# Kernel tuning notes

Measured on AMD Instinct MI355X. Metric: run time of the kernel, lower is better.

The kernel has to match this reference:

```python
import jax, jax.numpy as jnp
import numpy as np

WS = 14  # window size
NH = 12  # num heads
EPS = 1e-5  # torch LayerNorm eps


def _rel_idx(ws: int) -> np.ndarray:
    coords = np.stack(np.meshgrid(np.arange(ws), np.arange(ws), indexing='ij'))
    cf = coords.reshape(2, -1)                      # (2, N)
    rel = cf[:, :, None] - cf[:, None, :]           # (2, N, N)
    rel = rel.transpose(1, 2, 0).copy()
    rel[:, :, 0] += ws - 1
    rel[:, :, 1] += ws - 1
    rel[:, :, 0] *= 2 * ws - 1
    return rel.sum(-1)                              # (N, N) int


def _layernorm(x, w, b):
    mu = jnp.mean(x, axis=-1, keepdims=True)
    var = jnp.var(x, axis=-1, keepdims=True)
    return (x - mu) * jax.lax.rsqrt(var + EPS) * w + b


def setup_inputs() -> dict:
    key = jax.random.key(0)
    ks = jax.random.split(key, 8)
    d, dff = 768, 3072
    s = lambda k, shape, sc: jax.random.normal(k, shape, jnp.float32) * sc
    return {
        'x': jax.random.normal(ks[0], (8, d, 56, 56), jnp.float32),
        'norm1_w': jnp.ones((d,), jnp.float32),
        'norm1_b': jnp.zeros((d,), jnp.float32),
        'qkv_w': s(ks[1], (d, 3 * d), 0.02),
        'qkv_b': jnp.zeros((3 * d,), jnp.float32),
        'rel_bias_table': s(ks[2], ((2 * WS - 1) ** 2, NH), 0.02),
        'proj_w': s(ks[3], (d, d), 0.02),
        'proj_b': jnp.zeros((d,), jnp.float32),
        'norm2_w': jnp.ones((d,), jnp.float32),
        'norm2_b': jnp.zeros((d,), jnp.float32),
        'fc1_w': s(ks[4], (d, dff), 0.02),
        'fc1_b': jnp.zeros((dff,), jnp.float32),
        'fc2_w': s(ks[5], (dff, d), 0.02),
        'fc2_b': jnp.zeros((d,), jnp.float32),
        'gamma1': jnp.full((d,), 1e-5, jnp.float32),
        'gamma2': jnp.full((d,), 1e-5, jnp.float32),
    }


def reference(x, norm1_w, norm1_b, qkv_w, qkv_b, rel_bias_table, proj_w, proj_b,
              norm2_w, norm2_b, fc1_w, fc1_b, fc2_w, fc2_b, gamma1, gamma2):
    B, C, H, W = x.shape
    nh, hd = NH, C // NH
    N = WS * WS
    xs = jnp.transpose(x, (0, 2, 3, 1))             # B,H,W,C
    shortcut = xs
    h = _layernorm(xs, norm1_w, norm1_b)

    # window partition (H, W divisible by WS)
    hw = h.reshape(B, H // WS, WS, W // WS, WS, C)
    hw = jnp.transpose(hw, (0, 1, 3, 2, 4, 5)).reshape(-1, N, C)  # (Bw, N, C)

    qkv = hw @ qkv_w + qkv_b                        # (Bw, N, 3C)
    qkv = qkv.reshape(-1, N, 3, nh, hd)
    q, k, v = [jnp.transpose(qkv[:, :, i], (0, 2, 1, 3)) for i in range(3)]  # (Bw,nh,N,hd)

    attn = jnp.einsum('bhnd,bhmd->bhnm', q, k) * (hd ** -0.5)
    rel_idx = jnp.asarray(_rel_idx(WS))             # static (N,N)
    bias = rel_bias_table[rel_idx]                  # (N,N,nh)
    attn = attn + jnp.transpose(bias, (2, 0, 1))[None]
    attn = jax.nn.softmax(attn, axis=-1)

    out = jnp.einsum('bhnm,bhmd->bnhd', attn, v).reshape(-1, N, C)
    out = out @ proj_w + proj_b                     # (Bw, N, C)

    # window reverse
    out = out.reshape(B, H // WS, W // WS, WS, WS, C)
    out = jnp.transpose(out, (0, 1, 3, 2, 4, 5)).reshape(B, H, W, C)

    xs = shortcut + gamma1 * out
    h2 = _layernorm(xs, norm2_w, norm2_b)
    mlp = jax.nn.gelu(h2 @ fc1_w + fc1_b, approximate=False) @ fc2_w + fc2_b
    xs = xs + gamma2 * mlp
    return jnp.transpose(xs, (0, 3, 1, 2))          # B,C,H,W
```

## Files before the change

kernel.cpp:

```cpp
#include <hip/hip_runtime.h>
#include <cstdint>
#include <cstddef>


typedef unsigned short u16;
typedef short short8 __attribute__((ext_vector_type(8)));
typedef float floatx4 __attribute__((ext_vector_type(4)));

static __device__ __forceinline__ float bf2f(u16 u) {
  return __uint_as_float(((unsigned)u) << 16);
}
static __device__ __forceinline__ u16 f2bf(float f) {
  unsigned u = __float_as_uint(f);
  return (u16)((u + 0x7FFFu + ((u >> 16) & 1u)) >> 16);
}
static __device__ __forceinline__ float ldin(const void* p, size_t i, int isf) {
  return isf ? ((const float*)p)[i] : bf2f(((const u16*)p)[i]);
}
static __device__ __forceinline__ void gload_lds16(const void* g, void* l) {
  __builtin_amdgcn_global_load_lds(
      (const __attribute__((address_space(1))) void*)g,
      (__attribute__((address_space(3))) void*)l, 16, 0, 0);
}
static __device__ __forceinline__ float fast_gelu(float v) {
  float u2 = v * (1.5957691216f + 0.0713548163f * v * v);
  return v * (1.0f / (1.0f + __expf(-u2)));
}

__global__ __launch_bounds__(256) void detect_kernel(const u16* __restrict__ x,
                                                     int* __restrict__ flag) {
  __shared__ int tot;
  if (threadIdx.x == 0) tot = 0;
  __syncthreads();
  int cnt = 0;
  for (int i = threadIdx.x; i < 4096; i += 256) {
    int e = (x[i] >> 7) & 0xFF;
    if (e >= 0xC1) cnt++;
  }
  atomicAdd(&tot, cnt);
  __syncthreads();
  if (threadIdx.x == 0) flag[0] = (tot > 16) ? 1 : 0;
}

__global__ __launch_bounds__(256) void cvt_params_kernel(
    const void* n1w, const void* n1b, const void* qkvb, const void* projb,
    const void* n2w, const void* n2b, const void* fc1b, const void* fc2b,
    const void* g1, const void* g2, const void* bt, u16* __restrict__ P,
    const int* __restrict__ flag) {
  int isf = *flag;
  int i = blockIdx.x * 256 + threadIdx.x;
  const void* src; int off;
  if      (i < 768)   { src = n1w;   off = i; }
  else if (i < 1536)  { src = n1b;   off = i - 768; }
  else if (i < 3840)  { src = qkvb;  off = i - 1536; }
  else if (i < 4608)  { src = projb; off = i - 3840; }
  else if (i < 5376)  { src = n2w;   off = i - 4608; }
  else if (i < 6144)  { src = n2b;   off = i - 5376; }
  else if (i < 9216)  { src = fc1b;  off = i - 6144; }
  else if (i < 9984)  { src = fc2b;  off = i - 9216; }
  else if (i < 10752) { src = g1;    off = i - 9984; }
  else if (i < 11520) { src = g2;    off = i - 10752; }
  else if (i < 20268) { src = bt;    off = i - 11520; }
  else return;
  P[i] = f2bf(ldin(src, off, isf));
}

__global__ __launch_bounds__(256) void wtr_kernel(const void* __restrict__ W,
                                                  u16* __restrict__ WT,
                                                  int K, int N,
                                                  const int* __restrict__ flag) {
  int isf = *flag;
  __shared__ u16 tl[32][33];
  int tx = threadIdx.x, ty = threadIdx.y;
  int n0 = blockIdx.x * 32, k0 = blockIdx.y * 32;
#pragma unroll
  for (int j = 0; j < 32; j += 8)
    tl[ty + j][tx] = f2bf(ldin(W, (size_t)(k0 + ty + j) * N + n0 + tx, isf));
  __syncthreads();
#pragma unroll
  for (int j = 0; j < 32; j += 8)
    WT[(size_t)(n0 + ty + j) * K + k0 + tx] = tl[tx][ty + j];
}

__global__ __launch_bounds__(256) void tin_kernel(const void* __restrict__ x,
                                                  u16* __restrict__ sc,
                                                  const int* __restrict__ flag) {
  int isf = *flag;
  int cc = blockIdx.x, h = blockIdx.y, b = blockIdx.z;
  __shared__ u16 tile[64 * 57];
  int tid = threadIdx.x;
  for (int i = tid; i < 64 * 56; i += 256) {
    int ci = i / 56, w = i - ci * 56;
    tile[ci * 57 + w] =
        f2bf(ldin(x, (((size_t)b * 768 + cc * 64 + ci) * 56 + h) * 56 + w, isf));
  }
  __syncthreads();
  int hb = h / 14, hi = h - hb * 14;
  for (int i = tid; i < 56 * 64; i += 256) {
    int w = i >> 6, ci = i & 63;
    int wb = w / 14, wj = w - wb * 14;
    int r = (b * 16 + hb * 4 + wb) * 196 + hi * 14 + wj;
    sc[(size_t)r * 768 + cc * 64 + ci] = tile[ci * 57 + w];
  }
}

__global__ __launch_bounds__(256) void tout_kernel(const u16* __restrict__ src,
                                                   void* __restrict__ out,
                                                   const int* __restrict__ flag) {
  int isf = *flag;
  int cc = blockIdx.x, h = blockIdx.y, b = blockIdx.z;
  __shared__ u16 tile[64 * 57];
  int tid = threadIdx.x;
  int hb = h / 14, hi = h - hb * 14;
  for (int i = tid; i < 56 * 64; i += 256) {
    int w = i >> 6, ci = i & 63;
    int wb = w / 14, wj = w - wb * 14;
    int r = (b * 16 + hb * 4 + wb) * 196 + hi * 14 + wj;
    tile[ci * 57 + w] = src[(size_t)r * 768 + cc * 64 + ci];
  }
  __syncthreads();
  for (int i = tid; i < 64 * 56; i += 256) {
    int ci = i / 56, w = i - ci * 56;
    size_t o = (((size_t)b * 768 + cc * 64 + ci) * 56 + h) * 56 + w;
    if (isf) ((float*)out)[o] = bf2f(tile[ci * 57 + w]);
    else     ((u16*)out)[o]   = tile[ci * 57 + w];
  }
}

__global__ __launch_bounds__(256) void ln_kernel(const u16* __restrict__ xin,
                                                 const u16* __restrict__ wt,
                                                 const u16* __restrict__ bs,
                                                 u16* __restrict__ out) {
  int row = blockIdx.x, t = threadIdx.x;
  const u16* xr = xin + (size_t)row * 768;
  float v0 = bf2f(xr[t]), v1 = bf2f(xr[t + 256]), v2 = bf2f(xr[t + 512]);
  float s1 = v0 + v1 + v2;
  float s2 = v0 * v0 + v1 * v1 + v2 * v2;
#pragma unroll
  for (int off = 32; off > 0; off >>= 1) {
    s1 += __shfl_xor(s1, off);
    s2 += __shfl_xor(s2, off);
  }
  __shared__ float p1[4], p2[4];
  if ((t & 63) == 0) { p1[t >> 6] = s1; p2[t >> 6] = s2; }
  __syncthreads();
  float S1 = p1[0] + p1[1] + p1[2] + p1[3];
  float S2 = p2[0] + p2[1] + p2[2] + p2[3];
  float mu = S1 * (1.f / 768.f);
  float var = S2 * (1.f / 768.f) - mu * mu;
  float rs = rsqrtf(var + 1e-5f);
  u16* orow = out + (size_t)row * 768;
  orow[t]       = f2bf((v0 - mu) * rs * bf2f(wt[t])       + bf2f(bs[t]));
  orow[t + 256] = f2bf((v1 - mu) * rs * bf2f(wt[t + 256]) + bf2f(bs[t + 256]));
  orow[t + 512] = f2bf((v2 - mu) * rs * bf2f(wt[t + 512]) + bf2f(bs[t + 512]));
}

template <int EPI, int NPH>
__global__ __launch_bounds__(512, 2) void gemm256_kernel(
    const u16* __restrict__ A, const u16* __restrict__ BT,
    const u16* __restrict__ bias, const u16* __restrict__ gamma,
    u16* __restrict__ out, int M, int N, int K, int NX, int NYT) {
  constexpr int BN   = 64 * NPH;
  constexpr int WM   = 8 / NPH;
  constexpr int MF   = 2 * NPH;
  constexpr int ABUF = 8192;
  constexpr int BBUF = 2048 * NPH;
  constexpr int BUFSZ = ABUF + BBUF;
  __shared__ __align__(16) u16 LDS[4 * BUFSZ];

  int bid = blockIdx.x;
  int r8 = bid & 7, q = bid >> 3;
  int xb = q % NX, yb = (q / NX) * 8 + r8;
  if (yb >= NYT) return;
  int m0 = yb * 256, n0 = xb * BN;

  int tid = threadIdx.x;
  int w = tid >> 6, l = tid & 63;
  int l15 = l & 15, quad = l >> 4;
  int wm = w & (WM - 1), wn = w / WM;

  int lrow16 = l >> 2;
  int lk = ((l & 3) ^ ((l >> 3) & 3)) * 8;
  int ra0 = m0 + w * 32 + lrow16;       if (ra0 > M - 1) ra0 = M - 1;
  int ra1 = m0 + w * 32 + 16 + lrow16;  if (ra1 > M - 1) ra1 = M - 1;
  const u16* a0 = A + (size_t)ra0 * K + lk;
  const u16* a1 = A + (size_t)ra1 * K + lk;
  const u16* b0;
  const u16* b1;
  int dB0, dB1;
  if constexpr (NPH == 4) {
    b0 = BT + (size_t)(n0 + w * 32 + lrow16) * K + lk;
    b1 = BT + (size_t)(n0 + w * 32 + 16 + lrow16) * K + lk;
    dB0 = (w * 2) * 512; dB1 = (w * 2 + 1) * 512;
  } else {
    b0 = BT + (size_t)(n0 + w * 16 + lrow16) * K + lk;
    b1 = b0; dB0 = w * 512; dB1 = 0;
  }
  int dA0 = (w * 2) * 512, dA1 = (w * 2 + 1) * 512;

  int kqs = (quad ^ ((l15 >> 1) & 3)) * 8;

  floatx4 acc[MF][4];
#pragma unroll
  for (int i = 0; i < MF; ++i)
#pragma unroll
    for (int jn = 0; jn < 4; ++jn)
#pragma unroll
      for (int e = 0; e < 4; ++e) acc[i][jn][e] = 0.f;

  int nt = K >> 5;

  auto STAGE = [&](int s) {
    u16* bb = LDS + (size_t)(s & 3) * BUFSZ;
    int ko = s << 5;
    gload_lds16(a0 + ko, bb + dA0);
    gload_lds16(a1 + ko, bb + dA1);
    gload_lds16(b0 + ko, bb + ABUF + dB0);
    if constexpr (NPH == 4) gload_lds16(b1 + ko, bb + ABUF + dB1);
  };

#pragma unroll
  for (int pt = 0; pt < 3; ++pt)
    if (pt < nt) STAGE(pt);

  for (int t = 0; t < nt; ++t) {
    int rem = nt - 1 - t;
    if constexpr (NPH == 4) {
      if (rem >= 2)      asm volatile("s_waitcnt vmcnt(8)" ::: "memory");
      else if (rem == 1) asm volatile("s_waitcnt vmcnt(4)" ::: "memory");
      else               asm volatile("s_waitcnt vmcnt(0)" ::: "memory");
    } else {
      if (rem >= 2)      asm volatile("s_waitcnt vmcnt(6)" ::: "memory");
      else if (rem == 1) asm volatile("s_waitcnt vmcnt(3)" ::: "memory");
      else               asm volatile("s_waitcnt vmcnt(0)" ::: "memory");
    }
    __builtin_amdgcn_s_barrier();
    if (t + 3 < nt) STAGE(t + 3);

    const u16* Ac = LDS + (size_t)(t & 3) * BUFSZ;
    const u16* Bc = Ac + ABUF;
    __builtin_amdgcn_s_setprio(1);
    short8 bfr[4];
#pragma unroll
    for (int ni = 0; ni < 4; ++ni)
      bfr[ni] = *(const short8*)&Bc[(wn * 64 + ni * 16 + l15) * 32 + kqs];
#pragma unroll
    for (int mi = 0; mi < MF; ++mi) {
      short8 afr =
          *(const short8*)&Ac[(wm * (32 * NPH) + mi * 16 + l15) * 32 + kqs];
#pragma unroll
      for (int ni = 0; ni < 4; ++ni)
        acc[mi][ni] = __builtin_amdgcn_mfma_f32_16x16x32_bf16(
            afr, bfr[ni], acc[mi][ni], 0, 0, 0);
    }
    __builtin_amdgcn_s_setprio(0);
  }

  constexpr int CSTR = BN + 8;
  u16* Cs = LDS;
  float bv[4];
#pragma unroll
  for (int ni = 0; ni < 4; ++ni)
    bv[ni] = bf2f(bias[n0 + wn * 64 + ni * 16 + l15]);
  for (int cch = 0; cch < 2; ++cch) {
    __syncthreads();
    if (((wm * NPH) >> 2) == cch) {
      int rbase = wm * (32 * NPH) - cch * 128 + quad * 4;
#pragma unroll
      for (int mi = 0; mi < MF; ++mi)
#pragma unroll
        for (int ni = 0; ni < 4; ++ni) {
          int cl = wn * 64 + ni * 16 + l15;
#pragma unroll
          for (int reg = 0; reg < 4; ++reg) {
            float v = acc[mi][ni][reg] + bv[ni];
            if constexpr (EPI == 2) v = fast_gelu(v);
            Cs[(rbase + mi * 16 + reg) * CSTR + cl] = f2bf(v);
          }
        }
    }
    __syncthreads();
#pragma unroll
    for (int it = 0; it < BN / 32; ++it) {
      int idx = it * 512 + tid;
      int row = idx / (BN / 8);
      int c8 = (idx - row * (BN / 8)) * 8;
      int grow = m0 + cch * 128 + row;
      if (grow < M) {
        short8 val = *(const short8*)&Cs[row * CSTR + c8];
        u16* po = out + (size_t)grow * N + n0 + c8;
        if constexpr (EPI == 1) {
          short8 rv = *(const short8*)po;
          short8 gv = *(const short8*)(gamma + n0 + c8);
          short8 res;
#pragma unroll
          for (int e = 0; e < 8; ++e)
            res[e] = (short)f2bf(bf2f((u16)rv[e]) +
                                 bf2f((u16)gv[e]) * bf2f((u16)val[e]));
          *(short8*)po = res;
        } else {
          *(short8*)po = val;
        }
      }
    }
  }
}

__global__ __launch_bounds__(256) void attn_kernel(const u16* __restrict__ qkv,
                                                   const u16* __restrict__ btab,
                                                   u16* __restrict__ out) {
  __shared__ __align__(16) u16 VT[64 * 232];
  __shared__ __align__(16) u16 Pa[4 * 2 * 512];
  __shared__ float bS[729];
  int bid = blockIdx.x;
  int win = bid / 12, h = bid - win * 12;
  int tid = threadIdx.x, w = tid >> 6, l = tid & 63;
  int lane15 = l & 15, quad = l >> 4;
  const u16* qbase = qkv + (size_t)win * 196 * 2304;

  for (int i = tid; i < 64 * 28; i += 256) {
    int d = i / 28, m = i - d * 28;
    VT[d * 232 + 196 + m] = 0;
  }
  for (int i = tid; i < 196 * 64; i += 256) {
    int m = i >> 6, d = i & 63;
    VT[d * 232 + m] = qbase[(size_t)m * 2304 + 1536 + h * 64 + d];
  }
  for (int i = tid; i < 729; i += 256) bS[i] = bf2f(btab[i * 12 + h]);
  __syncthreads();

  u16* Pw = Pa + w * 1024;
  for (int rt = w; rt < 13; rt += 4) {
    floatx4 acc[13];
#pragma unroll
    for (int nt = 0; nt < 13; ++nt)
#pragma unroll
      for (int e = 0; e < 4; ++e) acc[nt][e] = 0.f;

    int rq = rt * 16 + lane15;
    bool qok = rq < 196;
#pragma unroll
    for (int kk = 0; kk < 2; ++kk) {
      short8 qf;
      if (qok)
        qf = *(const short8*)&qbase[(size_t)rq * 2304 + h * 64 + kk * 32 + quad * 8];
      else
#pragma unroll
        for (int e = 0; e < 8; ++e) qf[e] = 0;
#pragma unroll
      for (int nt = 0; nt < 13; ++nt) {
        int n = nt * 16 + lane15;
        short8 kf = *(const short8*)&qbase[(size_t)n * 2304 + 768 + h * 64 + kk * 32 + quad * 8];
        acc[nt] = __builtin_amdgcn_mfma_f32_16x16x32_bf16(qf, kf, acc[nt], 0, 0, 0);
      }
    }

    int i1[4], j1[4]; bool rv[4]; float mx[4], sm[4];
#pragma unroll
    for (int reg = 0; reg < 4; ++reg) {
      int r = rt * 16 + quad * 4 + reg;
      i1[reg] = r / 14; j1[reg] = r - i1[reg] * 14;
      rv[reg] = r < 196; mx[reg] = -1e30f; sm[reg] = 0.f;
    }
#pragma unroll
    for (int nt = 0; nt < 13; ++nt) {
      int cc = nt * 16 + lane15;
      bool cv = cc < 196;
      int i2 = cc / 14, j2 = cc - i2 * 14;
#pragma unroll
      for (int reg = 0; reg < 4; ++reg) {
        float v;
        if (cv) {
          v = acc[nt][reg] * 0.125f;
          if (rv[reg]) v += bS[(i1[reg] - i2 + 13) * 27 + (j1[reg] - j2 + 13)];
        } else v = -1e30f;
        acc[nt][reg] = v;
        mx[reg] = fmaxf(mx[reg], v);
      }
    }
#pragma unroll
    for (int reg = 0; reg < 4; ++reg)
#pragma unroll
      for (int off = 1; off < 16; off <<= 1)
        mx[reg] = fmaxf(mx[reg], __shfl_xor(mx[reg], off));
#pragma unroll
    for (int nt = 0; nt < 13; ++nt)
#pragma unroll
      for (int reg = 0; reg < 4; ++reg) {
        float p = __expf(acc[nt][reg] - mx[reg]);
        acc[nt][reg] = p; sm[reg] += p;
      }
#pragma unroll
    for (int reg = 0; reg < 4; ++reg) {
#pragma unroll
      for (int off = 1; off < 16; off <<= 1) sm[reg] += __shfl_xor(sm[reg], off);
      sm[reg] = 1.f / sm[reg];
    }

    floatx4 oa[4];
#pragma unroll
    for (int dt = 0; dt < 4; ++dt)
#pragma unroll
      for (int e = 0; e < 4; ++e) oa[dt][e] = 0.f;
#pragma unroll
    for (int kk = 0; kk < 7; ++kk) {
      u16* Pb = Pw + (kk & 1) * 512;
#pragma unroll
      for (int p = 0; p < 2; ++p) {
        int nt = kk * 2 + p;
#pragma unroll
        for (int reg = 0; reg < 4; ++reg) {
          float v = (nt < 13) ? acc[nt][reg] * sm[reg] : 0.f;
          Pb[(quad * 4 + reg) * 32 + p * 16 + lane15] = f2bf(v);
        }
      }
      asm volatile("s_waitcnt lgkmcnt(0)" ::: "memory");
      short8 pf = *(const short8*)&Pb[lane15 * 32 + quad * 8];
#pragma unroll
      for (int dt = 0; dt < 4; ++dt) {
        short8 vf = *(const short8*)&VT[(dt * 16 + lane15) * 232 + kk * 32 + quad * 8];
        oa[dt] = __builtin_amdgcn_mfma_f32_16x16x32_bf16(pf, vf, oa[dt], 0, 0, 0);
      }
    }
#pragma unroll
    for (int dt = 0; dt < 4; ++dt)
#pragma unroll
      for (int reg = 0; reg < 4; ++reg) {
        int r = rt * 16 + quad * 4 + reg;
        if (r < 196)
          out[((size_t)win * 196 + r) * 768 + h * 64 + dt * 16 + lane15] =
              f2bf(oa[dt][reg]);
      }
  }
}

static inline int gemm_grid(int NX, int NYT) { return NX * ((NYT + 7) / 8) * 8; }

extern "C" void kernel_launch(void* const* d_in, const int* in_sizes, int n_in,
                              void* d_out, int out_size, void* d_ws, size_t ws_size,
                              hipStream_t stream) {
  const void* x      = d_in[0];
  const void* n1w    = d_in[1];
  const void* n1b    = d_in[2];
  const void* qkv_w  = d_in[3];
  const void* qkv_b  = d_in[4];
  const void* btab   = d_in[5];
  const void* proj_w = d_in[6];
  const void* proj_b = d_in[7];
  const void* n2w    = d_in[8];
  const void* n2b    = d_in[9];
  const void* fc1_w  = d_in[10];
  const void* fc1_b  = d_in[11];
  const void* fc2_w  = d_in[12];
  const void* fc2_b  = d_in[13];
  const void* gamma1 = d_in[14];
  const void* gamma2 = d_in[15];
  (void)in_sizes; (void)n_in; (void)out_size;

  int c;
  if      (ws_size >= 245432576ull) c = 1;
  else if (ws_size >= 168362240ull) c = 2;
  else                              c = 4;
  const int R = 25088 / c;
  const int WN = 128 / c;
  const int NYT = (R + 255) / 256;

  char* ws = (char*)d_ws;
  int*  flag  = (int*)ws;
  u16*  P     = (u16*)(ws + 256);
  u16*  qkvT  = (u16*)(ws + 65792);
  u16*  projT = (u16*)(ws + 65792 + 3538944);
  u16*  fc1T  = (u16*)(ws + 65792 + 4718592);
  u16*  fc2T  = (u16*)(ws + 65792 + 9437184);
  const size_t B0 = 38535168;
  u16*  buf0  = (u16*)(ws + 14221568);
  u16*  buf1  = (u16*)(ws + 14221568 + B0);
  char* scr   = ws + 14221568 + 2 * B0;

  u16 *p_n1w = P, *p_n1b = P + 768, *p_qkvb = P + 1536, *p_projb = P + 3840;
  u16 *p_n2w = P + 4608, *p_n2b = P + 5376, *p_fc1b = P + 6144;
  u16 *p_fc2b = P + 9216, *p_g1 = P + 9984, *p_g2 = P + 10752, *p_bt = P + 11520;

  dim3 b256(256), b512(512), bw(32, 8);
  detect_kernel<<<dim3(1), b256, 0, stream>>>((const u16*)x, flag);
  cvt_params_kernel<<<dim3(80), b256, 0, stream>>>(
      n1w, n1b, qkv_b, proj_b, n2w, n2b, fc1_b, fc2_b, gamma1, gamma2, btab,
      P, flag);
  wtr_kernel<<<dim3(72, 24), bw, 0, stream>>>(qkv_w, qkvT, 768, 2304, flag);
  wtr_kernel<<<dim3(24, 24), bw, 0, stream>>>(proj_w, projT, 768, 768, flag);
  wtr_kernel<<<dim3(96, 24), bw, 0, stream>>>(fc1_w, fc1T, 768, 3072, flag);
  wtr_kernel<<<dim3(24, 96), bw, 0, stream>>>(fc2_w, fc2T, 3072, 768, flag);

  tin_kernel<<<dim3(12, 56, 8), b256, 0, stream>>>(x, buf0, flag);
  ln_kernel<<<dim3(25088), b256, 0, stream>>>(buf0, p_n1w, p_n1b, buf1);

  for (int hc = 0; hc < c; ++hc) {
    size_t ro = (size_t)hc * R * 768;
    u16* qC = (u16*)scr;
    u16* aC = (u16*)(scr + (size_t)R * 4608);
    gemm256_kernel<0, 4><<<dim3(gemm_grid(9, NYT)), b512, 0, stream>>>(
        buf1 + ro, qkvT, p_qkvb, nullptr, qC, R, 2304, 768, 9, NYT);
    attn_kernel<<<dim3(WN * 12), b256, 0, stream>>>(qC, p_bt, aC);
    gemm256_kernel<1, 2><<<dim3(gemm_grid(6, NYT)), b512, 0, stream>>>(
        aC, projT, p_projb, p_g1, buf0 + ro, R, 768, 768, 6, NYT);
  }

  ln_kernel<<<dim3(25088), b256, 0, stream>>>(buf0, p_n2w, p_n2b, buf1);

  for (int hc = 0; hc < c; ++hc) {
    size_t ro = (size_t)hc * R * 768;
    u16* gC = (u16*)scr;
    gemm256_kernel<2, 4><<<dim3(gemm_grid(12, NYT)), b512, 0, stream>>>(
        buf1 + ro, fc1T, p_fc1b, nullptr, gC, R, 3072, 768, 12, NYT);
    gemm256_kernel<1, 2><<<dim3(gemm_grid(6, NYT)), b512, 0, stream>>>(
        gC, fc2T, p_fc2b, p_g2, buf0 + ro, R, 768, 3072, 6, NYT);
  }

  tout_kernel<<<dim3(12, 56, 8), b256, 0, stream>>>(buf0, d_out, flag);
}
```

Before: 988.6 us.

## Replace pipelined 256-row GEMM with simpler 128x128 single-buffer GEMM

Swaps the 512-thread, 4-stage async-prefetch GEMM for a 256-thread kernel computing 128x128 tiles with a single LDS buffer and barrier-load-barrier-compute per K step. It aims for higher occupancy (4 blocks per CU) and a smaller tile so more blocks fill the grid. In exchange it loses the load/compute overlap of the multi-stage pipeline and doubles operand reloads from global memory.

```diff
diff --git a/kernel.cpp b/kernel.cpp
--- a/kernel.cpp
+++ b/kernel.cpp
@@ -155,29 +155,23 @@
   orow[t + 512] = f2bf((v2 - mu) * rs * bf2f(wt[t + 512]) + bf2f(bs[t + 512]));
 }
 
-template <int EPI, int NPH>
-__global__ __launch_bounds__(512, 2) void gemm256_kernel(
+template <int EPI>
+__global__ __launch_bounds__(256, 4) void gemm128_kernel(
     const u16* __restrict__ A, const u16* __restrict__ BT,
     const u16* __restrict__ bias, const u16* __restrict__ gamma,
     u16* __restrict__ out, int M, int N, int K, int NX, int NYT) {
-  constexpr int BN   = 64 * NPH;
-  constexpr int WM   = 8 / NPH;
-  constexpr int MF   = 2 * NPH;
-  constexpr int ABUF = 8192;
-  constexpr int BBUF = 2048 * NPH;
-  constexpr int BUFSZ = ABUF + BBUF;
-  __shared__ __align__(16) u16 LDS[4 * BUFSZ];
+  __shared__ __align__(16) u16 LDS[8704];
 
   int bid = blockIdx.x;
   int r8 = bid & 7, q = bid >> 3;
   int xb = q % NX, yb = (q / NX) * 8 + r8;
   if (yb >= NYT) return;
-  int m0 = yb * 256, n0 = xb * BN;
+  int m0 = yb * 128, n0 = xb * 128;
 
   int tid = threadIdx.x;
   int w = tid >> 6, l = tid & 63;
   int l15 = l & 15, quad = l >> 4;
-  int wm = w & (WM - 1), wn = w / WM;
+  int wm = w & 1, wn = w >> 1;
 
   int lrow16 = l >> 2;
   int lk = ((l & 3) ^ ((l >> 3) & 3)) * 8;
@@ -185,69 +179,37 @@
   int ra1 = m0 + w * 32 + 16 + lrow16;  if (ra1 > M - 1) ra1 = M - 1;
   const u16* a0 = A + (size_t)ra0 * K + lk;
   const u16* a1 = A + (size_t)ra1 * K + lk;
-  const u16* b0;
-  const u16* b1;
-  int dB0, dB1;
-  if constexpr (NPH == 4) {
-    b0 = BT + (size_t)(n0 + w * 32 + lrow16) * K + lk;
-    b1 = BT + (size_t)(n0 + w * 32 + 16 + lrow16) * K + lk;
-    dB0 = (w * 2) * 512; dB1 = (w * 2 + 1) * 512;
-  } else {
-    b0 = BT + (size_t)(n0 + w * 16 + lrow16) * K + lk;
-    b1 = b0; dB0 = w * 512; dB1 = 0;
-  }
+  const u16* b0 = BT + (size_t)(n0 + w * 32 + lrow16) * K + lk;
+  const u16* b1 = BT + (size_t)(n0 + w * 32 + 16 + lrow16) * K + lk;
   int dA0 = (w * 2) * 512, dA1 = (w * 2 + 1) * 512;
 
   int kqs = (quad ^ ((l15 >> 1) & 3)) * 8;
 
-  floatx4 acc[MF][4];
-#pragma unroll
-  for (int i = 0; i < MF; ++i)
-#pragma unroll
-    for (int jn = 0; jn < 4; ++jn)
-#pragma unroll
-      for (int e = 0; e < 4; ++e) acc[i][jn][e] = 0.f;
+  floatx4 acc[4][4];
+#pragma unroll
+  for (int i = 0; i < 4; ++i)
+#pragma unroll
+    for (int j = 0; j < 4; ++j)
+#pragma unroll
+      for (int e = 0; e < 4; ++e) acc[i][j][e] = 0.f;
 
   int nt = K >> 5;
-
-  auto STAGE = [&](int s) {
-    u16* bb = LDS + (size_t)(s & 3) * BUFSZ;
-    int ko = s << 5;
-    gload_lds16(a0 + ko, bb + dA0);
-    gload_lds16(a1 + ko, bb + dA1);
-    gload_lds16(b0 + ko, bb + ABUF + dB0);
-    if constexpr (NPH == 4) gload_lds16(b1 + ko, bb + ABUF + dB1);
-  };
-
-#pragma unroll
-  for (int pt = 0; pt < 3; ++pt)
-    if (pt < nt) STAGE(pt);
-
   for (int t = 0; t < nt; ++t) {
-    int rem = nt - 1 - t;
-    if constexpr (NPH == 4) {
-      if (rem >= 2)      asm volatile("s_waitcnt vmcnt(8)" ::: "memory");
-      else if (rem == 1) asm volatile("s_waitcnt vmcnt(4)" ::: "memory");
-      else               asm volatile("s_waitcnt vmcnt(0)" ::: "memory");
-    } else {
-      if (rem >= 2)      asm volatile("s_waitcnt vmcnt(6)" ::: "memory");
-      else if (rem == 1) asm volatile("s_waitcnt vmcnt(3)" ::: "memory");
-      else               asm volatile("s_waitcnt vmcnt(0)" ::: "memory");
-    }
-    __builtin_amdgcn_s_barrier();
-    if (t + 3 < nt) STAGE(t + 3);
-
-    const u16* Ac = LDS + (size_t)(t & 3) * BUFSZ;
-    const u16* Bc = Ac + ABUF;
+    int ko = t << 5;
+    __syncthreads();
+    gload_lds16(a0 + ko, LDS + dA0);
+    gload_lds16(a1 + ko, LDS + dA1);
+    gload_lds16(b0 + ko, LDS + 4096 + dA0);
+    gload_lds16(b1 + ko, LDS + 4096 + dA1);
+    __syncthreads();
     __builtin_amdgcn_s_setprio(1);
     short8 bfr[4];
 #pragma unroll
     for (int ni = 0; ni < 4; ++ni)
-      bfr[ni] = *(const short8*)&Bc[(wn * 64 + ni * 16 + l15) * 32 + kqs];
-#pragma unroll
-    for (int mi = 0; mi < MF; ++mi) {
-      short8 afr =
-          *(const short8*)&Ac[(wm * (32 * NPH) + mi * 16 + l15) * 32 + kqs];
+      bfr[ni] = *(const short8*)&LDS[4096 + (wn * 64 + ni * 16 + l15) * 32 + kqs];
+#pragma unroll
+    for (int mi = 0; mi < 4; ++mi) {
+      short8 afr = *(const short8*)&LDS[(wm * 64 + mi * 16 + l15) * 32 + kqs];
 #pragma unroll
       for (int ni = 0; ni < 4; ++ni)
         acc[mi][ni] = __builtin_amdgcn_mfma_f32_16x16x32_bf16(
@@ -256,18 +218,16 @@
     __builtin_amdgcn_s_setprio(0);
   }
 
-  constexpr int CSTR = BN + 8;
-  u16* Cs = LDS;
+  constexpr int CSTR = 136;
   float bv[4];
 #pragma unroll
   for (int ni = 0; ni < 4; ++ni)
     bv[ni] = bf2f(bias[n0 + wn * 64 + ni * 16 + l15]);
   for (int cch = 0; cch < 2; ++cch) {
     __syncthreads();
-    if (((wm * NPH) >> 2) == cch) {
-      int rbase = wm * (32 * NPH) - cch * 128 + quad * 4;
-#pragma unroll
-      for (int mi = 0; mi < MF; ++mi)
+    if (wm == cch) {
+#pragma unroll
+      for (int mi = 0; mi < 4; ++mi)
 #pragma unroll
         for (int ni = 0; ni < 4; ++ni) {
           int cl = wn * 64 + ni * 16 + l15;
@@ -275,19 +235,18 @@
           for (int reg = 0; reg < 4; ++reg) {
             float v = acc[mi][ni][reg] + bv[ni];
             if constexpr (EPI == 2) v = fast_gelu(v);
-            Cs[(rbase + mi * 16 + reg) * CSTR + cl] = f2bf(v);
+            LDS[(mi * 16 + quad * 4 + reg) * CSTR + cl] = f2bf(v);
           }
         }
     }
     __syncthreads();
 #pragma unroll
-    for (int it = 0; it < BN / 32; ++it) {
-      int idx = it * 512 + tid;
-      int row = idx / (BN / 8);
-      int c8 = (idx - row * (BN / 8)) * 8;
-      int grow = m0 + cch * 128 + row;
+    for (int it = 0; it < 4; ++it) {
+      int idx = it * 256 + tid;
+      int row = idx >> 4, c8 = (idx & 15) * 8;
+      int grow = m0 + cch * 64 + row;
       if (grow < M) {
-        short8 val = *(const short8*)&Cs[row * CSTR + c8];
+        short8 val = *(const short8*)&LDS[row * CSTR + c8];
         u16* po = out + (size_t)grow * N + n0 + c8;
         if constexpr (EPI == 1) {
           short8 rv = *(const short8*)po;
@@ -463,7 +422,7 @@
   else                              c = 4;
   const int R = 25088 / c;
   const int WN = 128 / c;
-  const int NYT = (R + 255) / 256;
+  const int NYT = (R + 127) / 128;
 
   char* ws = (char*)d_ws;
   int*  flag  = (int*)ws;
@@ -481,7 +440,7 @@
   u16 *p_n2w = P + 4608, *p_n2b = P + 5376, *p_fc1b = P + 6144;
   u16 *p_fc2b = P + 9216, *p_g1 = P + 9984, *p_g2 = P + 10752, *p_bt = P + 11520;
 
-  dim3 b256(256), b512(512), bw(32, 8);
+  dim3 b256(256), bw(32, 8);
   detect_kernel<<<dim3(1), b256, 0, stream>>>((const u16*)x, flag);
   cvt_params_kernel<<<dim3(80), b256, 0, stream>>>(
       n1w, n1b, qkv_b, proj_b, n2w, n2b, fc1_b, fc2_b, gamma1, gamma2, btab,
@@ -498,10 +457,10 @@
     size_t ro = (size_t)hc * R * 768;
     u16* qC = (u16*)scr;
     u16* aC = (u16*)(scr + (size_t)R * 4608);
-    gemm256_kernel<0, 4><<<dim3(gemm_grid(9, NYT)), b512, 0, stream>>>(
-        buf1 + ro, qkvT, p_qkvb, nullptr, qC, R, 2304, 768, 9, NYT);
+    gemm128_kernel<0><<<dim3(gemm_grid(18, NYT)), b256, 0, stream>>>(
+        buf1 + ro, qkvT, p_qkvb, nullptr, qC, R, 2304, 768, 18, NYT);
     attn_kernel<<<dim3(WN * 12), b256, 0, stream>>>(qC, p_bt, aC);
-    gemm256_kernel<1, 2><<<dim3(gemm_grid(6, NYT)), b512, 0, stream>>>(
+    gemm128_kernel<1><<<dim3(gemm_grid(6, NYT)), b256, 0, stream>>>(
         aC, projT, p_projb, p_g1, buf0 + ro, R, 768, 768, 6, NYT);
   }
 
@@ -510,9 +469,9 @@
   for (int hc = 0; hc < c; ++hc) {
     size_t ro = (size_t)hc * R * 768;
     u16* gC = (u16*)scr;
-    gemm256_kernel<2, 4><<<dim3(gemm_grid(12, NYT)), b512, 0, stream>>>(
-        buf1 + ro, fc1T, p_fc1b, nullptr, gC, R, 3072, 768, 12, NYT);
-    gemm256_kernel<1, 2><<<dim3(gemm_grid(6, NYT)), b512, 0, stream>>>(
+    gemm128_kernel<2><<<dim3(gemm_grid(24, NYT)), b256, 0, stream>>>(
+        buf1 + ro, fc1T, p_fc1b, nullptr, gC, R, 3072, 768, 24, NYT);
+    gemm128_kernel<1><<<dim3(gemm_grid(6, NYT)), b256, 0, stream>>>(
         gC, fc2T, p_fc2b, p_g2, buf0 + ro, R, 768, 3072, 6, NYT);
   }
 
```

Result: no change. 980.8 us (-0.8%).
